# Kernel optimization log

Hardware: AMD Instinct MI355X
Metric: run time of the kernel (lower is better)

The kernel has to match this reference:

```python
import jax, jax.numpy as jnp
import numpy as np

D_MODEL = 1024
D_FFN = 2048
WINDOW = 64
EPS = 1e-6


def rmsnorm(x, w):
    rms = jnp.sqrt(jnp.mean(x * x, axis=-1, keepdims=True) + EPS)
    return x / rms * w


def setup_inputs() -> dict:
    key = jax.random.key(0)
    ks = jax.random.split(key, 9)
    s = 0.02
    return {
        "x": jax.random.normal(ks[0], (4, 2048, D_MODEL), dtype=jnp.float32),
        "norm1_w": jnp.ones((D_MODEL,), dtype=jnp.float32),
        "norm2_w": jnp.ones((D_MODEL,), dtype=jnp.float32),
        "Wq": jax.random.normal(ks[1], (D_MODEL, D_MODEL), dtype=jnp.float32) * s,
        "Wk": jax.random.normal(ks[2], (D_MODEL, D_MODEL), dtype=jnp.float32) * s,
        "Wv": jax.random.normal(ks[3], (D_MODEL, D_MODEL), dtype=jnp.float32) * s,
        "Wo": jax.random.normal(ks[4], (D_MODEL, D_MODEL), dtype=jnp.float32) * s,
        "W1": jax.random.normal(ks[5], (D_MODEL, D_FFN), dtype=jnp.float32) * s,
        "W2": jax.random.normal(ks[6], (D_FFN, D_MODEL), dtype=jnp.float32) * s,
        "W3": jax.random.normal(ks[7], (D_MODEL, D_FFN), dtype=jnp.float32) * s,
    }


def reference(x, norm1_w, norm2_w, Wq, Wk, Wv, Wo, W1, W2, W3):
    B, T, D = x.shape
    scale = D ** (-0.5)
    residual = x
    xn = rmsnorm(x, norm1_w)
    q = xn @ Wq  # [B,T,D]
    k = xn @ Wk
    v = xn @ Wv
    # causal local-window mask: attend iff 0 <= i-j < WINDOW
    rows = jnp.arange(T)[:, None]
    cols = jnp.arange(T)[None, :]
    mask = (cols <= rows) & (rows - cols < WINDOW)  # [T,T] bool
    scores = jnp.einsum("bid,bjd->bij", q, k) * scale
    scores = jnp.where(mask[None], scores, -jnp.inf)
    weights = jax.nn.softmax(scores, axis=-1)
    attended = jnp.einsum("bij,bjd->bid", weights, v)
    x = residual + attended @ Wo
    # SwiGLU FFN
    xn2 = rmsnorm(x, norm2_w)
    ffn = (jax.nn.silu(xn2 @ W1) * (xn2 @ W3)) @ W2
    return x + ffn
```

## Files before the change

kernel.cpp:

```cpp
#include <hip/hip_runtime.h>
#include <hip/hip_bf16.h>

typedef __attribute__((ext_vector_type(8))) short bf16x8;
typedef __attribute__((ext_vector_type(4))) float f32x4;

__device__ __forceinline__ short to_bf16s(float f) {
    union { __hip_bfloat16 h; short s; } u;
    u.h = __float2bfloat16(f);
    return u.s;
}

__device__ __forceinline__ void load_lds16(const void* g, void* l) {
    __builtin_amdgcn_global_load_lds((const __attribute__((address_space(1))) void*)g,
                                     (__attribute__((address_space(3))) void*)l, 16, 0, 0);
}

__global__ __launch_bounds__(256)
void transpose_all(const float* __restrict__ Wq, const float* __restrict__ Wk,
                   const float* __restrict__ Wv, const float* __restrict__ Wo,
                   const float* __restrict__ W1, const float* __restrict__ W3,
                   const float* __restrict__ W2,
                   short* __restrict__ WqT, short* __restrict__ WkT,
                   short* __restrict__ WvT, short* __restrict__ WoT,
                   short* __restrict__ W13T, short* __restrict__ W2T) {
    __shared__ float tile[32][33];
    const int bid = blockIdx.x;
    const float* src; short* dst; int K, N, tl, rs = 1, ro = 0;
    if (bid < 4096) {
        const int wi = bid >> 10; tl = bid & 1023;
        src = wi == 0 ? Wq : wi == 1 ? Wk : wi == 2 ? Wv : Wo;
        dst = wi == 0 ? WqT : wi == 1 ? WkT : wi == 2 ? WvT : WoT;
        K = 1024; N = 1024;
    } else if (bid < 8192) {
        const int wi = (bid - 4096) >> 11; tl = (bid - 4096) & 2047;
        src = wi ? W3 : W1; dst = W13T; rs = 2; ro = wi;
        K = 1024; N = 2048;
    } else {
        tl = bid - 8192; src = W2; dst = W2T;
        K = 2048; N = 1024;
    }
    const int nx = N >> 5;
    const int n0 = (tl % nx) * 32, k0 = (tl / nx) * 32;
    const int t = threadIdx.x;
    {
        const int lr = t >> 3, lc = (t & 7) * 4;
        float4 v = *(const float4*)&src[(long)(k0 + lr) * N + n0 + lc];
        tile[lr][lc] = v.x; tile[lr][lc + 1] = v.y;
        tile[lr][lc + 2] = v.z; tile[lr][lc + 3] = v.w;
    }
    __syncthreads();
    {
        const int nr = t >> 3, kc = (t & 7) * 4;
        short4 o;
        o.x = to_bf16s(tile[kc][nr]);
        o.y = to_bf16s(tile[kc + 1][nr]);
        o.z = to_bf16s(tile[kc + 2][nr]);
        o.w = to_bf16s(tile[kc + 3][nr]);
        *(short4*)&dst[(long)((n0 + nr) * rs + ro) * K + k0 + kc] = o;
    }
}

__global__ __launch_bounds__(256)
void rmsnorm_kernel(const float* __restrict__ x, const float* __restrict__ wt,
                    short* __restrict__ out) {
    const int D = 1024;
    const long row = blockIdx.x;
    const int t = threadIdx.x;
    float4 v = ((const float4*)(x + row * D))[t];
    float ss = v.x * v.x + v.y * v.y + v.z * v.z + v.w * v.w;
    #pragma unroll
    for (int off = 32; off; off >>= 1) ss += __shfl_xor(ss, off);
    __shared__ float red[4];
    if ((t & 63) == 0) red[t >> 6] = ss;
    __syncthreads();
    ss = red[0] + red[1] + red[2] + red[3];
    const float inv = rsqrtf(ss * (1.0f / 1024.0f) + 1e-6f);
    float4 wv = ((const float4*)wt)[t];
    short4 o;
    o.x = to_bf16s(v.x * inv * wv.x);
    o.y = to_bf16s(v.y * inv * wv.y);
    o.z = to_bf16s(v.z * inv * wv.z);
    o.w = to_bf16s(v.w * inv * wv.w);
    *(short4*)&out[row * D + t * 4] = o;
}

#define MFMA16(MB, NB, BREG)                                                   \
    __builtin_amdgcn_s_barrier();                                              \
    asm volatile("s_waitcnt lgkmcnt(0)");                                      \
    __builtin_amdgcn_s_setprio(1);                                             \
    _Pragma("unroll")                                                          \
    for (int m_ = 0; m_ < 4; ++m_)                                             \
        _Pragma("unroll")                                                      \
        for (int n_ = 0; n_ < 2; ++n_) {                                       \
            acc[(MB) + m_][(NB) + n_] = __builtin_amdgcn_mfma_f32_16x16x32_bf16( \
                a[m_][0], BREG[n_][0], acc[(MB) + m_][(NB) + n_], 0, 0, 0);    \
            acc[(MB) + m_][(NB) + n_] = __builtin_amdgcn_mfma_f32_16x16x32_bf16( \
                a[m_][1], BREG[n_][1], acc[(MB) + m_][(NB) + n_], 0, 0, 0);    \
        }                                                                      \
    __builtin_amdgcn_s_setprio(0);                                             \
    __builtin_amdgcn_s_barrier();

#define RA1(BUF)                                                               \
    _Pragma("unroll")                                                          \
    for (int m_ = 0; m_ < 4; ++m_) {                                           \
        const int rb_ = (BUF) * 32768 + (wr * 64 + m_ * 16 + lm) * 128;        \
        a[m_][0] = *(const bf16x8*)&lds[rb_ + ((lk * 16) ^ sw)];               \
        a[m_][1] = *(const bf16x8*)&lds[rb_ + ((64 + lk * 16) ^ sw)];          \
    }
#define RB1(BUF, NG, ARR)                                                      \
    _Pragma("unroll")                                                          \
    for (int n_ = 0; n_ < 2; ++n_) {                                           \
        const int rb_ = 98304 + (BUF) * 16384 +                                \
                        (wc * 64 + ((NG) * 2 + n_) * 16 + lm) * 128;           \
        ARR[n_][0] = *(const bf16x8*)&lds[rb_ + ((lk * 16) ^ sw)];             \
        ARR[n_][1] = *(const bf16x8*)&lds[rb_ + ((64 + lk * 16) ^ sw)];        \
    }

template<int EPI>
__global__ __launch_bounds__(512, 2)
void gemm128r(const short* __restrict__ A, const short* __restrict__ B0,
              const float* __restrict__ res, void* __restrict__ outp,
              short* __restrict__ outp2, int M, int N, int K) {
    __shared__ __align__(16) char lds[147456];

    const int t = threadIdx.x;
    const int lane = t & 63, w = t >> 6;
    const int wr = w >> 1, wc = w & 1;
    const int lm = lane & 15, lk = lane >> 4;
    const int sw = (lm & 7) << 4;

    const int nbn = N >> 7;
    const int chunk = gridDim.x >> 3;
    const int logical = (blockIdx.x & 7) * chunk + (blockIdx.x >> 3);
    const int bm = logical / nbn, bn = logical - (logical / nbn) * nbn;

    const long Kb = (long)K * 2;
    const char* Ab = (const char*)A;
    const char* Bb = (const char*)B0;

    long srcA[2][2], srcB[2];
    {
        const int rowp = t >> 3;
        const int cbx = (t & 7) * 16;
        const int swz = ((t >> 3) & 7) << 4;
        #pragma unroll
        for (int h = 0; h < 2; ++h)
            #pragma unroll
            for (int c = 0; c < 2; ++c)
                srcA[h][c] = (long)(bm * 256 + h * 128 + c * 64 + rowp) * Kb + (cbx ^ swz);
        #pragma unroll
        for (int c = 0; c < 2; ++c)
            srcB[c] = (long)(bn * 128 + c * 64 + rowp) * Kb + (cbx ^ swz);
    }
    auto stA = [&](int kt, int h, int buf) {
        #pragma unroll
        for (int c = 0; c < 2; ++c)
            load_lds16(Ab + srcA[h][c] + (long)kt * 128,
                       &lds[buf * 32768 + h * 16384 + c * 8192 + t * 16]);
    };
    auto stB = [&](int kt, int buf) {
        #pragma unroll
        for (int c = 0; c < 2; ++c)
            load_lds16(Bb + srcB[c] + (long)kt * 128,
                       &lds[98304 + buf * 16384 + c * 8192 + t * 16]);
    };

    f32x4 acc[4][4] = {};
    bf16x8 a[4][2], b0[2][2], b1[2][2];
    const int nt = K >> 6;

    stA(0, 0, 0); stA(0, 1, 0); stB(0, 0);
    stA(1, 0, 1); stA(1, 1, 1); stB(1, 1);
    asm volatile("s_waitcnt vmcnt(6)" ::: "memory");
    __builtin_amdgcn_s_barrier();

    int cur = 0, stg = 2;
    for (int kt = 0; kt < nt; ++kt) {
        const bool pf = (kt + 2) < nt;
        RA1(cur); RB1(cur, 0, b0);
        if (pf) { stA(kt + 2, 0, stg); stA(kt + 2, 1, stg); }
        MFMA16(0, 0, b0)
        RB1(cur, 1, b1);
        if (pf) stB(kt + 2, stg);
        if (kt + 1 < nt) asm volatile("s_waitcnt vmcnt(6)" ::: "memory");
        else             asm volatile("s_waitcnt vmcnt(0)" ::: "memory");
        MFMA16(0, 2, b1)
        cur = (cur == 2) ? 0 : cur + 1;
        stg = (stg == 2) ? 0 : stg + 1;
    }

    #pragma unroll
    for (int mf = 0; mf < 4; ++mf)
      #pragma unroll
      for (int nf = 0; nf < 4; ++nf)
        #pragma unroll
        for (int r = 0; r < 4; ++r) {
            const int grow = bm * 256 + wr * 64 + mf * 16 + lk * 4 + r;
            const int gcol = bn * 128 + wc * 64 + nf * 16 + lm;
            const float v = acc[mf][nf][r];
            if constexpr (EPI == 2) {
                const long i = (long)grow * N + gcol;
                ((float*)outp)[i] = res[i] + v;
            } else {
                if (gcol < 2048)
                    ((short*)outp)[(long)grow * 2048 + gcol] = to_bf16s(v);
                else
                    outp2[(long)(gcol - 2048) * 8192 + grow] = to_bf16s(v);
            }
        }
}

#define RA2(BUF, MG)                                                           \
    _Pragma("unroll")                                                          \
    for (int m_ = 0; m_ < 4; ++m_) {                                           \
        const int rb_ = ((BUF) * 2 + wr) * 16384 + (((MG) * 4 + m_) * 16 + lm) * 128; \
        a[m_][0] = *(const bf16x8*)&lds[rb_ + ((lk * 16) ^ sw)];               \
        a[m_][1] = *(const bf16x8*)&lds[rb_ + ((64 + lk * 16) ^ sw)];          \
    }
#define RB2(BUF, NH, ARR)                                                      \
    _Pragma("unroll")                                                          \
    for (int n_ = 0; n_ < 2; ++n_) {                                           \
        const int rb_ = 65536 + ((BUF) * 2 + (wc >> 1)) * 16384 +              \
                        ((wc & 1) * 64 + ((NH) * 2 + n_) * 16 + lm) * 128;     \
        ARR[n_][0] = *(const bf16x8*)&lds[rb_ + ((lk * 16) ^ sw)];             \
        ARR[n_][1] = *(const bf16x8*)&lds[rb_ + ((64 + lk * 16) ^ sw)];        \
    }

__global__ __launch_bounds__(512, 2)
void gemm256f(const short* __restrict__ A, const short* __restrict__ B0,
              short* __restrict__ outp, int M, int N, int K) {
    __shared__ __align__(16) char lds[131072];

    const int t = threadIdx.x;
    const int lane = t & 63, w = t >> 6;
    const int wr = w >> 2, wc = w & 3;
    const int lm = lane & 15, lk = lane >> 4;
    const int sw = (lm & 7) << 4;

    const int nbn = N >> 8;
    const int chunk = gridDim.x >> 3;
    const int logical = (blockIdx.x & 7) * chunk + (blockIdx.x >> 3);
    const int bm = logical / nbn, bn = logical - (logical / nbn) * nbn;

    const long Kb = (long)K * 2;
    const char* Ab = (const char*)A;
    const char* Bb = (const char*)B0;

    long srcA[2][2], srcB[2][2];
    {
        const int rowp = t >> 3;
        const int cbx = (t & 7) * 16;
        const int swz = ((t >> 3) & 7) << 4;
        #pragma unroll
        for (int h = 0; h < 2; ++h)
            #pragma unroll
            for (int c = 0; c < 2; ++c) {
                srcA[h][c] = (long)(bm * 256 + h * 128 + c * 64 + rowp) * Kb + (cbx ^ swz);
                srcB[h][c] = (long)(bn * 256 + h * 128 + c * 64 + rowp) * Kb + (cbx ^ swz);
            }
    }
    auto stA = [&](int kt, int h) {
        const int buf = kt & 1;
        #pragma unroll
        for (int c = 0; c < 2; ++c)
            load_lds16(Ab + srcA[h][c] + (long)kt * 128,
                       &lds[(buf * 2 + h) * 16384 + c * 8192 + t * 16]);
    };
    auto stB = [&](int kt, int h) {
        const int buf = kt & 1;
        #pragma unroll
        for (int c = 0; c < 2; ++c)
            load_lds16(Bb + srcB[h][c] + (long)kt * 128,
                       &lds[65536 + (buf * 2 + h) * 16384 + c * 8192 + t * 16]);
    };

    f32x4 acc[8][4] = {};
    bf16x8 a[4][2], b0[2][2], b1[2][2];
    const int nt = K >> 6;

    stB(0, 0); stB(0, 1); stA(0, 0); stA(0, 1); stB(1, 0); stB(1, 1);
    asm volatile("s_waitcnt vmcnt(4)" ::: "memory");
    __builtin_amdgcn_s_barrier();

    for (int u = 0; u < nt; u += 2) {
        const bool pf = (u + 2) < nt;
        RA2(0, 0); RB2(0, 0, b0);
        stA(u + 1, 0);
        MFMA16(0, 0, b0)
        RB2(0, 1, b1);
        stA(u + 1, 1);
        MFMA16(0, 2, b1)
        RA2(0, 1);
        if (pf) stB(u + 2, 0);
        MFMA16(4, 2, b1)
        if (pf) { stB(u + 2, 1); asm volatile("s_waitcnt vmcnt(4)" ::: "memory"); }
        else    { asm volatile("s_waitcnt vmcnt(0)" ::: "memory"); }
        MFMA16(4, 0, b0)
        RA2(1, 0); RB2(1, 0, b0);
        if (pf) stA(u + 2, 0);
        MFMA16(0, 0, b0)
        RB2(1, 1, b1);
        if (pf) stA(u + 2, 1);
        MFMA16(0, 2, b1)
        RA2(1, 1);
        if (pf) stB(u + 3, 0);
        MFMA16(4, 2, b1)
        if (pf) { stB(u + 3, 1); asm volatile("s_waitcnt vmcnt(4)" ::: "memory"); }
        else    { asm volatile("s_waitcnt vmcnt(0)" ::: "memory"); }
        MFMA16(4, 0, b0)
    }

    const int NH = N >> 1;
    #pragma unroll
    for (int mf = 0; mf < 8; ++mf)
      #pragma unroll
      for (int nf = 0; nf < 4; ++nf)
        #pragma unroll
        for (int r = 0; r < 4; ++r) {
            const int grow = bm * 256 + wr * 128 + mf * 16 + lk * 4 + r;
            const int gcol = bn * 256 + wc * 64 + nf * 16 + lm;
            const float v = acc[mf][nf][r];
            const float g3 = __shfl_xor(v, 1);
            if (!(lane & 1)) {
                const float sws = v / (1.f + __expf(-v));
                outp[(long)grow * NH + (gcol >> 1)] = to_bf16s(sws * g3);
            }
        }
}

__global__ __launch_bounds__(128)
void attn_kernel(const short* __restrict__ Q, const short* __restrict__ Km,
                 int ldq, const short* __restrict__ VT, short* __restrict__ att) {
    const int T = 2048, D = 1024, Mtot = 8192;
    const int bid = blockIdx.x;
    const int b = bid >> 6;
    const int q0 = (bid & 63) << 5;
    const long qrow0 = (long)b * T + q0;
    const int t = threadIdx.x, lane = t & 63, w = t >> 6;

    __shared__ short Qs[2][32 * 32];
    __shared__ short Ks[2][96 * 32];
    __shared__ float S_lds[32][100];
    __shared__ short P_lds[32 * 96];
    __shared__ short VTs[2][128 * 96];

    const int trow = t >> 2, tk8 = (t & 3) * 8;
    auto stageQK = [&](int kt, int bf) {
        const int k0 = kt << 5;
        load_lds16(Q + (qrow0 + trow) * ldq + k0 + tk8, &Qs[bf][t * 8]);
        #pragma unroll
        for (int s2 = 0; s2 < 3; ++s2) {
            const int krow = s2 * 32 + trow;
            int j = q0 - 64 + krow; if (j < 0) j = 0;
            load_lds16(Km + ((long)b * T + j) * ldq + k0 + tk8, &Ks[bf][(s2 * 128 + t) * 8]);
        }
    };

    f32x4 s[6] = {};
    stageQK(0, 0);
    __syncthreads();
    for (int kt = 0; kt < 32; ++kt) {
        const int cb = kt & 1;
        if (kt + 1 < 32) stageQK(kt + 1, cb ^ 1);
        const int ko = (lane >> 4) * 8;
        const bf16x8 aq = *(const bf16x8*)&Qs[cb][(w * 16 + (lane & 15)) * 32 + ko];
        #pragma unroll
        for (int n = 0; n < 6; ++n) {
            const bf16x8 bk = *(const bf16x8*)&Ks[cb][(n * 16 + (lane & 15)) * 32 + ko];
            s[n] = __builtin_amdgcn_mfma_f32_16x16x32_bf16(aq, bk, s[n], 0, 0, 0);
        }
        __syncthreads();
    }
    #pragma unroll
    for (int n = 0; n < 6; ++n)
        #pragma unroll
        for (int r = 0; r < 4; ++r)
            S_lds[w * 16 + ((lane >> 4) << 2) + r][n * 16 + (lane & 15)] = s[n][r] * 0.03125f;
    __syncthreads();

    {
        const int row = t >> 2, c0 = (t & 3) * 24;
        float e[24];
        float mx = -1e30f;
        #pragma unroll
        for (int c = 0; c < 24; ++c) {
            const int kj = c0 + c;
            const bool valid = (kj > row) && (kj <= row + 64) && (q0 - 64 + kj >= 0);
            const float sv = valid ? S_lds[row][kj] : -1e30f;
            e[c] = sv;
            mx = fmaxf(mx, sv);
        }
        mx = fmaxf(mx, __shfl_xor(mx, 1));
        mx = fmaxf(mx, __shfl_xor(mx, 2));
        float sum = 0.f;
        #pragma unroll
        for (int c = 0; c < 24; ++c) {
            const float ev = (e[c] > -1e29f) ? __expf(e[c] - mx) : 0.f;
            e[c] = ev; sum += ev;
        }
        sum += __shfl_xor(sum, 1);
        sum += __shfl_xor(sum, 2);
        const float inv = 1.f / sum;
        #pragma unroll
        for (int c = 0; c < 24; ++c)
            P_lds[row * 96 + c0 + c] = to_bf16s(e[c] * inv);
    }

    auto stageV = [&](int dc, int bf) {
        #pragma unroll
        for (int s2 = 0; s2 < 12; ++s2) {
            const int idx = s2 * 128 + t;
            const int dr = idx / 12, c = idx - dr * 12;
            int j = q0 - 64 + c * 8; if (j < 0) j = 0;
            load_lds16(VT + (long)(dc * 128 + dr) * Mtot + b * T + j, &VTs[bf][idx * 8]);
        }
    };
    stageV(0, 0);
    __syncthreads();

    bf16x8 pa[3];
    {
        const int ko = (lane >> 4) * 8;
        #pragma unroll
        for (int kc = 0; kc < 3; ++kc)
            pa[kc] = *(const bf16x8*)&P_lds[(w * 16 + (lane & 15)) * 96 + kc * 32 + ko];
    }
    for (int dc = 0; dc < 8; ++dc) {
        const int cb = dc & 1;
        if (dc + 1 < 8) stageV(dc + 1, cb ^ 1);
        f32x4 o[8] = {};
        const int ko = (lane >> 4) * 8;
        #pragma unroll
        for (int kc = 0; kc < 3; ++kc)
            #pragma unroll
            for (int n = 0; n < 8; ++n) {
                const bf16x8 vb = *(const bf16x8*)&VTs[cb][(n * 16 + (lane & 15)) * 96 + kc * 32 + ko];
                o[n] = __builtin_amdgcn_mfma_f32_16x16x32_bf16(pa[kc], vb, o[n], 0, 0, 0);
            }
        __syncthreads();
        #pragma unroll
        for (int n = 0; n < 8; ++n)
            #pragma unroll
            for (int r = 0; r < 4; ++r) {
                const long grow = qrow0 + w * 16 + ((lane >> 4) << 2) + r;
                const int gcol = dc * 128 + n * 16 + (lane & 15);
                att[grow * D + gcol] = to_bf16s(o[n][r]);
            }
    }
}

extern "C" void kernel_launch(void* const* d_in, const int* in_sizes, int n_in,
                              void* d_out, int out_size, void* d_ws, size_t ws_size,
                              hipStream_t stream) {
    const float* x   = (const float*)d_in[0];
    const float* n1w = (const float*)d_in[1];
    const float* n2w = (const float*)d_in[2];
    const float* Wq  = (const float*)d_in[3];
    const float* Wk  = (const float*)d_in[4];
    const float* Wv  = (const float*)d_in[5];
    const float* Wo  = (const float*)d_in[6];
    const float* W1  = (const float*)d_in[7];
    const float* W2  = (const float*)d_in[8];
    const float* W3  = (const float*)d_in[9];

    const int M = 8192;
    char* ws = (char*)d_ws;
    size_t off = 0;
    auto alloc = [&](size_t bytes) { void* p = ws + off; off += (bytes + 255) & ~(size_t)255; return p; };

    short* xn1 = (short*)alloc((size_t)M * 1024 * 2);
    short* qk  = (short*)alloc((size_t)M * 2048 * 2);
    short* vT  = (short*)alloc((size_t)M * 1024 * 2);
    float* x2  = (float*)alloc((size_t)M * 1024 * 4);
    short* WqT = (short*)alloc((size_t)1024 * 1024 * 2);
    short* WkT = (short*)alloc((size_t)1024 * 1024 * 2);
    short* WvT = (short*)alloc((size_t)1024 * 1024 * 2);
    short* WoT = (short*)alloc((size_t)1024 * 1024 * 2);
    short* W13T= (short*)alloc((size_t)4096 * 1024 * 2);
    short* W2T = (short*)alloc((size_t)1024 * 2048 * 2);
    short* att = xn1;
    short* xn2 = qk;
    short* h   = qk + (size_t)M * 1024;

    transpose_all<<<10240, 256, 0, stream>>>(Wq, Wk, Wv, Wo, W1, W3, W2,
                                             WqT, WkT, WvT, WoT, W13T, W2T);

    rmsnorm_kernel<<<M, 256, 0, stream>>>(x, n1w, xn1);
    gemm128r<5><<<768, 512, 0, stream>>>(xn1, WqT, nullptr, qk, vT, M, 3072, 1024);
    attn_kernel<<<256, 128, 0, stream>>>(qk, qk + 1024, 2048, vT, att);
    gemm128r<2><<<256, 512, 0, stream>>>(att, WoT, x, x2, nullptr, M, 1024, 1024);
    rmsnorm_kernel<<<M, 256, 0, stream>>>(x2, n2w, xn2);
    gemm256f<<<512, 512, 0, stream>>>(xn2, W13T, h, M, 4096, 1024);
    gemm128r<2><<<256, 512, 0, stream>>>(h, W2T, x2, (float*)d_out, nullptr, M, 1024, 2048);
}
```

Before: 305.0 us.

## Fuse rmsnorm into weight prep, double-buffer QKV GEMM, add 128x128 output GEMM

The first rmsnorm moves into the weight-transpose kernel as extra blocks, which removes one launch. The QKV GEMM changes from a triple-buffered to a double-buffered LDS pipeline with a smaller footprint (96KB instead of 144KB), meant to improve occupancy. The Wo and W2 projections now use a new 128x128-tile, 256-thread GEMM with 512 blocks instead of 256 for better CU coverage. The new kernel uses a simple synchronous double-buffer schedule, so load latency may be hidden less well.

```diff
diff --git a/kernel.cpp b/kernel.cpp
--- a/kernel.cpp
+++ b/kernel.cpp
@@ -16,15 +16,38 @@
 }
 
 __global__ __launch_bounds__(256)
-void transpose_all(const float* __restrict__ Wq, const float* __restrict__ Wk,
-                   const float* __restrict__ Wv, const float* __restrict__ Wo,
-                   const float* __restrict__ W1, const float* __restrict__ W3,
-                   const float* __restrict__ W2,
-                   short* __restrict__ WqT, short* __restrict__ WkT,
-                   short* __restrict__ WvT, short* __restrict__ WoT,
-                   short* __restrict__ W13T, short* __restrict__ W2T) {
+void prep_kernel(const float* __restrict__ Wq, const float* __restrict__ Wk,
+                 const float* __restrict__ Wv, const float* __restrict__ Wo,
+                 const float* __restrict__ W1, const float* __restrict__ W3,
+                 const float* __restrict__ W2,
+                 short* __restrict__ WqT, short* __restrict__ WkT,
+                 short* __restrict__ WvT, short* __restrict__ WoT,
+                 short* __restrict__ W13T, short* __restrict__ W2T,
+                 const float* __restrict__ x, const float* __restrict__ n1w,
+                 short* __restrict__ xn1) {
+    const int bid = blockIdx.x;
+    const int t = threadIdx.x;
+    if (bid >= 10240) {
+        const long row = bid - 10240;
+        float4 v = ((const float4*)(x + row * 1024))[t];
+        float ss = v.x * v.x + v.y * v.y + v.z * v.z + v.w * v.w;
+        #pragma unroll
+        for (int off = 32; off; off >>= 1) ss += __shfl_xor(ss, off);
+        __shared__ float red[4];
+        if ((t & 63) == 0) red[t >> 6] = ss;
+        __syncthreads();
+        ss = red[0] + red[1] + red[2] + red[3];
+        const float inv = rsqrtf(ss * (1.0f / 1024.0f) + 1e-6f);
+        float4 wv = ((const float4*)n1w)[t];
+        short4 o;
+        o.x = to_bf16s(v.x * inv * wv.x);
+        o.y = to_bf16s(v.y * inv * wv.y);
+        o.z = to_bf16s(v.z * inv * wv.z);
+        o.w = to_bf16s(v.w * inv * wv.w);
+        *(short4*)&xn1[row * 1024 + t * 4] = o;
+        return;
+    }
     __shared__ float tile[32][33];
-    const int bid = blockIdx.x;
     const float* src; short* dst; int K, N, tl, rs = 1, ro = 0;
     if (bid < 4096) {
         const int wi = bid >> 10; tl = bid & 1023;
@@ -41,7 +64,6 @@
     }
     const int nx = N >> 5;
     const int n0 = (tl % nx) * 32, k0 = (tl / nx) * 32;
-    const int t = threadIdx.x;
     {
         const int lr = t >> 3, lc = (t & 7) * 4;
         float4 v = *(const float4*)&src[(long)(k0 + lr) * N + n0 + lc];
@@ -63,10 +85,9 @@
 __global__ __launch_bounds__(256)
 void rmsnorm_kernel(const float* __restrict__ x, const float* __restrict__ wt,
                     short* __restrict__ out) {
-    const int D = 1024;
     const long row = blockIdx.x;
     const int t = threadIdx.x;
-    float4 v = ((const float4*)(x + row * D))[t];
+    float4 v = ((const float4*)(x + row * 1024))[t];
     float ss = v.x * v.x + v.y * v.y + v.z * v.z + v.w * v.w;
     #pragma unroll
     for (int off = 32; off; off >>= 1) ss += __shfl_xor(ss, off);
@@ -81,7 +102,7 @@
     o.y = to_bf16s(v.y * inv * wv.y);
     o.z = to_bf16s(v.z * inv * wv.z);
     o.w = to_bf16s(v.w * inv * wv.w);
-    *(short4*)&out[row * D + t * 4] = o;
+    *(short4*)&out[row * 1024 + t * 4] = o;
 }
 
 #define MFMA16(MB, NB, BREG)                                                   \
@@ -100,28 +121,28 @@
     __builtin_amdgcn_s_setprio(0);                                             \
     __builtin_amdgcn_s_barrier();
 
-#define RA1(BUF)                                                               \
+#define QRA(BUF)                                                               \
     _Pragma("unroll")                                                          \
     for (int m_ = 0; m_ < 4; ++m_) {                                           \
-        const int rb_ = (BUF) * 32768 + (wr * 64 + m_ * 16 + lm) * 128;        \
+        const int rb_ = ((BUF) * 2 + (wr >> 1)) * 16384 +                      \
+                        ((wr & 1) * 64 + m_ * 16 + lm) * 128;                  \
         a[m_][0] = *(const bf16x8*)&lds[rb_ + ((lk * 16) ^ sw)];               \
         a[m_][1] = *(const bf16x8*)&lds[rb_ + ((64 + lk * 16) ^ sw)];          \
     }
-#define RB1(BUF, NG, ARR)                                                      \
+#define QRB(BUF, NG, ARR)                                                      \
     _Pragma("unroll")                                                          \
     for (int n_ = 0; n_ < 2; ++n_) {                                           \
-        const int rb_ = 98304 + (BUF) * 16384 +                                \
-                        (wc * 64 + ((NG) * 2 + n_) * 16 + lm) * 128;           \
+        const int rb_ = 65536 + ((BUF) * 2 + wc) * 8192 +                      \
+                        (((NG) * 2 + n_) * 16 + lm) * 128;                     \
         ARR[n_][0] = *(const bf16x8*)&lds[rb_ + ((lk * 16) ^ sw)];             \
         ARR[n_][1] = *(const bf16x8*)&lds[rb_ + ((64 + lk * 16) ^ sw)];        \
     }
 
-template<int EPI>
 __global__ __launch_bounds__(512, 2)
-void gemm128r(const short* __restrict__ A, const short* __restrict__ B0,
-              const float* __restrict__ res, void* __restrict__ outp,
-              short* __restrict__ outp2, int M, int N, int K) {
-    __shared__ __align__(16) char lds[147456];
+void gemm256qkv(const short* __restrict__ A, const short* __restrict__ B0,
+                short* __restrict__ outp, short* __restrict__ outp2,
+                int M, int N, int K) {
+    __shared__ __align__(16) char lds[98304];
 
     const int t = threadIdx.x;
     const int lane = t & 63, w = t >> 6;
@@ -149,44 +170,49 @@
             for (int c = 0; c < 2; ++c)
                 srcA[h][c] = (long)(bm * 256 + h * 128 + c * 64 + rowp) * Kb + (cbx ^ swz);
         #pragma unroll
-        for (int c = 0; c < 2; ++c)
-            srcB[c] = (long)(bn * 128 + c * 64 + rowp) * Kb + (cbx ^ swz);
-    }
-    auto stA = [&](int kt, int h, int buf) {
+        for (int h = 0; h < 2; ++h)
+            srcB[h] = (long)(bn * 128 + h * 64 + rowp) * Kb + (cbx ^ swz);
+    }
+    auto stA = [&](int kt, int h) {
+        const int buf = kt & 1;
         #pragma unroll
         for (int c = 0; c < 2; ++c)
             load_lds16(Ab + srcA[h][c] + (long)kt * 128,
-                       &lds[buf * 32768 + h * 16384 + c * 8192 + t * 16]);
+                       &lds[(buf * 2 + h) * 16384 + c * 8192 + t * 16]);
     };
-    auto stB = [&](int kt, int buf) {
-        #pragma unroll
-        for (int c = 0; c < 2; ++c)
-            load_lds16(Bb + srcB[c] + (long)kt * 128,
-                       &lds[98304 + buf * 16384 + c * 8192 + t * 16]);
+    auto stB = [&](int kt, int h) {
+        const int buf = kt & 1;
+        load_lds16(Bb + srcB[h] + (long)kt * 128,
+                   &lds[65536 + (buf * 2 + h) * 8192 + t * 16]);
     };
 
     f32x4 acc[4][4] = {};
     bf16x8 a[4][2], b0[2][2], b1[2][2];
     const int nt = K >> 6;
 
-    stA(0, 0, 0); stA(0, 1, 0); stB(0, 0);
-    stA(1, 0, 1); stA(1, 1, 1); stB(1, 1);
+    stA(0, 0); stA(0, 1); stB(0, 0); stB(0, 1);
+    stA(1, 0); stA(1, 1); stB(1, 0); stB(1, 1);
     asm volatile("s_waitcnt vmcnt(6)" ::: "memory");
     __builtin_amdgcn_s_barrier();
 
-    int cur = 0, stg = 2;
-    for (int kt = 0; kt < nt; ++kt) {
-        const bool pf = (kt + 2) < nt;
-        RA1(cur); RB1(cur, 0, b0);
-        if (pf) { stA(kt + 2, 0, stg); stA(kt + 2, 1, stg); }
+    for (int u = 0; u < nt; u += 2) {
+        const bool pf = (u + 2) < nt;
+        QRA(0); QRB(0, 0, b0);
+        if (pf) stA(u + 2, 0);
         MFMA16(0, 0, b0)
-        RB1(cur, 1, b1);
-        if (pf) stB(kt + 2, stg);
-        if (kt + 1 < nt) asm volatile("s_waitcnt vmcnt(6)" ::: "memory");
-        else             asm volatile("s_waitcnt vmcnt(0)" ::: "memory");
+        QRB(0, 1, b1);
+        if (pf) { stA(u + 2, 1); stB(u + 2, 0); stB(u + 2, 1);
+                  asm volatile("s_waitcnt vmcnt(6)" ::: "memory"); }
+        else    { asm volatile("s_waitcnt vmcnt(0)" ::: "memory"); }
         MFMA16(0, 2, b1)
-        cur = (cur == 2) ? 0 : cur + 1;
-        stg = (stg == 2) ? 0 : stg + 1;
+        QRA(1); QRB(1, 0, b0);
+        if (pf) stA(u + 3, 0);
+        MFMA16(0, 0, b0)
+        QRB(1, 1, b1);
+        if (pf) { stA(u + 3, 1); stB(u + 3, 0); stB(u + 3, 1);
+                  asm volatile("s_waitcnt vmcnt(6)" ::: "memory"); }
+        else    { asm volatile("s_waitcnt vmcnt(0)" ::: "memory"); }
+        MFMA16(0, 2, b1)
     }
 
     #pragma unroll
@@ -198,15 +224,99 @@
             const int grow = bm * 256 + wr * 64 + mf * 16 + lk * 4 + r;
             const int gcol = bn * 128 + wc * 64 + nf * 16 + lm;
             const float v = acc[mf][nf][r];
-            if constexpr (EPI == 2) {
-                const long i = (long)grow * N + gcol;
-                ((float*)outp)[i] = res[i] + v;
-            } else {
-                if (gcol < 2048)
-                    ((short*)outp)[(long)grow * 2048 + gcol] = to_bf16s(v);
-                else
-                    outp2[(long)(gcol - 2048) * 8192 + grow] = to_bf16s(v);
+            if (gcol < 2048)
+                outp[(long)grow * 2048 + gcol] = to_bf16s(v);
+            else
+                outp2[(long)(gcol - 2048) * 8192 + grow] = to_bf16s(v);
+        }
+}
+
+__global__ __launch_bounds__(256, 2)
+void gemm128o(const short* __restrict__ A, const short* __restrict__ B0,
+              const float* __restrict__ res, float* __restrict__ outp,
+              int M, int N, int K) {
+    __shared__ __align__(16) char lds[65536];
+
+    const int t = threadIdx.x;
+    const int lane = t & 63, w = t >> 6;
+    const int wr = w >> 1, wc = w & 1;
+    const int lm = lane & 15, lk = lane >> 4;
+    const int sw = (lm & 7) << 4;
+
+    const int nbn = N >> 7;
+    const int chunk = gridDim.x >> 3;
+    const int logical = (blockIdx.x & 7) * chunk + (blockIdx.x >> 3);
+    const int bm = logical / nbn, bn = logical - (logical / nbn) * nbn;
+
+    const long Kb = (long)K * 2;
+    const char* Ab = (const char*)A;
+    const char* Bb = (const char*)B0;
+
+    long srcA[4], srcB[4];
+    {
+        const int rowp = t >> 3;
+        const int cbx = (t & 7) * 16;
+        const int swz = ((t >> 3) & 7) << 4;
+        #pragma unroll
+        for (int c = 0; c < 4; ++c) {
+            srcA[c] = (long)(bm * 128 + c * 32 + rowp) * Kb + (cbx ^ swz);
+            srcB[c] = (long)(bn * 128 + c * 32 + rowp) * Kb + (cbx ^ swz);
+        }
+    }
+    auto stage = [&](int kt, int buf) {
+        #pragma unroll
+        for (int c = 0; c < 4; ++c)
+            load_lds16(Ab + srcA[c] + (long)kt * 128,
+                       &lds[buf * 16384 + c * 4096 + t * 16]);
+        #pragma unroll
+        for (int c = 0; c < 4; ++c)
+            load_lds16(Bb + srcB[c] + (long)kt * 128,
+                       &lds[32768 + buf * 16384 + c * 4096 + t * 16]);
+    };
+
+    f32x4 acc[4][4] = {};
+    const int nt = K >> 6;
+
+    stage(0, 0);
+    asm volatile("s_waitcnt vmcnt(0)" ::: "memory");
+    __syncthreads();
+
+    for (int kt = 0; kt < nt; ++kt) {
+        const int buf = kt & 1;
+        if (kt + 1 < nt) stage(kt + 1, buf ^ 1);
+        bf16x8 a[4][2], b[4][2];
+        #pragma unroll
+        for (int m = 0; m < 4; ++m) {
+            const int rb = buf * 16384 + (wr * 64 + m * 16 + lm) * 128;
+            a[m][0] = *(const bf16x8*)&lds[rb + ((lk * 16) ^ sw)];
+            a[m][1] = *(const bf16x8*)&lds[rb + ((64 + lk * 16) ^ sw)];
+        }
+        #pragma unroll
+        for (int n = 0; n < 4; ++n) {
+            const int rb = 32768 + buf * 16384 + (wc * 64 + n * 16 + lm) * 128;
+            b[n][0] = *(const bf16x8*)&lds[rb + ((lk * 16) ^ sw)];
+            b[n][1] = *(const bf16x8*)&lds[rb + ((64 + lk * 16) ^ sw)];
+        }
+        #pragma unroll
+        for (int m = 0; m < 4; ++m)
+            #pragma unroll
+            for (int n = 0; n < 4; ++n) {
+                acc[m][n] = __builtin_amdgcn_mfma_f32_16x16x32_bf16(a[m][0], b[n][0], acc[m][n], 0, 0, 0);
+                acc[m][n] = __builtin_amdgcn_mfma_f32_16x16x32_bf16(a[m][1], b[n][1], acc[m][n], 0, 0, 0);
             }
+        __syncthreads();
+    }
+
+    #pragma unroll
+    for (int m = 0; m < 4; ++m)
+      #pragma unroll
+      for (int n = 0; n < 4; ++n)
+        #pragma unroll
+        for (int r = 0; r < 4; ++r) {
+            const int grow = bm * 128 + wr * 64 + m * 16 + lk * 4 + r;
+            const int gcol = bn * 128 + wc * 64 + n * 16 + lm;
+            const long i = (long)grow * N + gcol;
+            outp[i] = res[i] + acc[m][n][r];
         }
 }
 
@@ -482,14 +592,13 @@
     short* xn2 = qk;
     short* h   = qk + (size_t)M * 1024;
 
-    transpose_all<<<10240, 256, 0, stream>>>(Wq, Wk, Wv, Wo, W1, W3, W2,
-                                             WqT, WkT, WvT, WoT, W13T, W2T);
-
-    rmsnorm_kernel<<<M, 256, 0, stream>>>(x, n1w, xn1);
-    gemm128r<5><<<768, 512, 0, stream>>>(xn1, WqT, nullptr, qk, vT, M, 3072, 1024);
+    prep_kernel<<<18432, 256, 0, stream>>>(Wq, Wk, Wv, Wo, W1, W3, W2,
+                                           WqT, WkT, WvT, WoT, W13T, W2T,
+                                           x, n1w, xn1);
+    gemm256qkv<<<768, 512, 0, stream>>>(xn1, WqT, qk, vT, M, 3072, 1024);
     attn_kernel<<<256, 128, 0, stream>>>(qk, qk + 1024, 2048, vT, att);
-    gemm128r<2><<<256, 512, 0, stream>>>(att, WoT, x, x2, nullptr, M, 1024, 1024);
+    gemm128o<<<512, 256, 0, stream>>>(att, WoT, x, x2, M, 1024, 1024);
     rmsnorm_kernel<<<M, 256, 0, stream>>>(x2, n2w, xn2);
     gemm256f<<<512, 512, 0, stream>>>(xn2, W13T, h, M, 4096, 1024);
-    gemm128r<2><<<256, 512, 0, stream>>>(h, W2T, x2, (float*)d_out, nullptr, M, 1024, 2048);
-}
+    gemm128o<<<512, 256, 0, stream>>>(h, W2T, x2, (float*)d_out, M, 1024, 2048);
+}
```

Result: no change. 299.2 us (-1.9%).
